# Kernel optimization log

Hardware: AMD Instinct MI355X
Metric: run time of the kernel (lower is better)

Reference implementation:

```python
import jax, jax.numpy as jnp
import numpy as np
import math

NH, NKV, D = 32, 8, 128  # query heads, kv heads, head_dim
ROPE_THETA = 10000.0


def _rotate_half(x):
    x1, x2 = jnp.split(x, 2, axis=-1)
    return jnp.concatenate([-x2, x1], axis=-1)


def _rope_cache(position_ids):
    # position_ids: [B, S] int -> cos, sin: [B, S, D]
    inv_freq = 1.0 / (ROPE_THETA ** (jnp.arange(0, D, 2, dtype=jnp.float32) / D))
    freqs = position_ids.astype(jnp.float32)[..., None] * inv_freq  # [B,S,D/2]
    emb = jnp.concatenate([freqs, freqs], axis=-1)  # [B,S,D]
    return jnp.cos(emb), jnp.sin(emb)


def setup_inputs() -> dict:
    key = jax.random.key(0)
    k0, k1, k2, k3, k4 = jax.random.split(key, 5)
    B, S, H = 1, 2048, 4096
    scale = 0.02
    return {
        "hidden_states": jax.random.normal(k0, (B, S, H), jnp.float32),
        "position_ids": jnp.broadcast_to(jnp.arange(S, dtype=jnp.int32), (B, S)),
        "Wq": jax.random.normal(k1, (H, NH * D), jnp.float32) * scale,
        "Wk": jax.random.normal(k2, (H, NKV * D), jnp.float32) * scale,
        "Wv": jax.random.normal(k3, (H, NKV * D), jnp.float32) * scale,
        "Wo": jax.random.normal(k4, (NH * D, H), jnp.float32) * scale,
    }


def reference(hidden_states, position_ids, Wq, Wk, Wv, Wo):
    B, S, H = hidden_states.shape
    # QKV projections, move heads front: [B, H, S, D]
    Q = (hidden_states @ Wq).reshape(B, S, NH, D).transpose(0, 2, 1, 3)
    K = (hidden_states @ Wk).reshape(B, S, NKV, D).transpose(0, 2, 1, 3)
    V = (hidden_states @ Wv).reshape(B, S, NKV, D).transpose(0, 2, 1, 3)
    # RoPE
    cos, sin = _rope_cache(position_ids)  # [B,S,D]
    cos, sin = cos[:, None], sin[:, None]  # broadcast over heads
    Q = Q * cos + _rotate_half(Q) * sin
    K = K * cos + _rotate_half(K) * sin
    # GQA: repeat kv heads to match query heads
    g = NH // NKV
    K = jnp.repeat(K, g, axis=1)
    V = jnp.repeat(V, g, axis=1)
    # scaled QK^T with causal mask (mask=True -> keep, else finfo.min)
    scores = jnp.einsum("bhqd,bhkd->bhqk", Q, K) / math.sqrt(D)
    causal = jnp.tril(jnp.ones((S, S), dtype=bool))
    scores = jnp.where(causal, scores, jnp.finfo(scores.dtype).min)
    probs = jax.nn.softmax(scores.astype(jnp.float32), axis=-1).astype(Q.dtype)
    attn = jnp.einsum("bhqk,bhkd->bhqd", probs, V)
    attn = attn.transpose(0, 2, 1, 3).reshape(B, S, NH * D)
    return attn @ Wo
```

## Files before the change

kernel.cpp:

```cpp
#include <hip/hip_runtime.h>
#include <hip/hip_bf16.h>
#include <math.h>

typedef __bf16 bf16;
typedef __bf16 bf16x4 __attribute__((ext_vector_type(4)));
typedef __bf16 bf16x8 __attribute__((ext_vector_type(8)));
typedef float f32x4 __attribute__((ext_vector_type(4)));

#define GLB __attribute__((address_space(1)))
#define LDSAS __attribute__((address_space(3)))

__global__ void probe_dtype(const unsigned int* __restrict__ X, int* __restrict__ flag) {
  int t = threadIdx.x;
  int cnt = 0;
  for (int i = t; i < 512; i += 64) {
    unsigned int e = (X[i] >> 7) & 0xFF;
    cnt += (e >= 110 && e <= 135) ? 1 : 0;
  }
#pragma unroll
  for (int off = 32; off > 0; off >>= 1) cnt += __shfl_down(cnt, off, 64);
  if (t == 0) flag[0] = (cnt < 256) ? 1 : 0;
}

__global__ void prep_weights(const void* __restrict__ Wq, const void* __restrict__ Wk,
                             const void* __restrict__ Wv, const void* __restrict__ Wo,
                             const void* __restrict__ X,
                             bf16* __restrict__ Wqkvt, bf16* __restrict__ Wot,
                             bf16* __restrict__ Xb, const int* __restrict__ flag) {
  const int f = flag[0];
  const int t = threadIdx.x;
  int b = blockIdx.x;
  __shared__ __attribute__((aligned(16))) bf16 tileT[64][72];
  const void* W;
  bf16* out;
  int N, bx, by;
  if (b < 4096) {
    W = Wq; out = Wqkvt; N = 4096; bx = b & 63; by = b >> 6;
  } else if (b < 5120) {
    b -= 4096; W = Wk; out = Wqkvt + (size_t)4096 * 4096; N = 1024; bx = b & 15; by = b >> 4;
  } else if (b < 6144) {
    b -= 5120; W = Wv; out = Wqkvt + (size_t)5120 * 4096; N = 1024; bx = b & 15; by = b >> 4;
  } else if (b < 10240) {
    b -= 6144; W = Wo; out = Wot; N = 4096; bx = b & 63; by = b >> 6;
  } else {
    b -= 10240;
    const size_t i = ((size_t)b * 256 + t) * 4;
    bf16x4 o;
    if (f) {
      const float4 v = *(const float4*)((const float*)X + i);
      o[0] = (bf16)v.x; o[1] = (bf16)v.y; o[2] = (bf16)v.z; o[3] = (bf16)v.w;
    } else {
      o = *(const bf16x4*)((const bf16*)X + i);
    }
    *(bf16x4*)&Xb[i] = o;
    return;
  }
  const int n0 = bx * 64, k0 = by * 64;

  const int rr = t >> 4, cc = (t & 15) * 4;
  const int s_in = (t & 15) >> 1;
#pragma unroll
  for (int p = 0; p < 4; ++p) {
    const int r = p * 16 + rr;
    bf16 vals[4];
    if (f) {
      const float4 v = *(const float4*)((const float*)W + (size_t)(k0 + r) * N + n0 + cc);
      vals[0] = (bf16)v.x; vals[1] = (bf16)v.y; vals[2] = (bf16)v.z; vals[3] = (bf16)v.w;
    } else {
      const bf16x4 v = *(const bf16x4*)((const bf16*)W + (size_t)(k0 + r) * N + n0 + cc);
#pragma unroll
      for (int u = 0; u < 4; ++u) vals[u] = v[u];
    }
    const int idx = (((r >> 3) ^ s_in) << 3) + (r & 7);
#pragma unroll
    for (int u = 0; u < 4; ++u) tileT[cc + u][idx] = vals[u];
  }
  __syncthreads();

  const int nn = t >> 3, c8 = t & 7;
#pragma unroll
  for (int p = 0; p < 2; ++p) {
    const int n = p * 32 + nn;
    const int s = (n >> 3) & 7;
    const bf16x8 v = *(const bf16x8*)&tileT[n][(c8 ^ s) * 8];
    *(bf16x8*)&out[(size_t)(n0 + n) * 4096 + k0 + c8 * 8] = v;
  }
}

__global__ __launch_bounds__(256, 2) void gemm_bt(
    const bf16* __restrict__ A, const bf16* __restrict__ Bt,
    void* __restrict__ C, const int* __restrict__ flagp, int M, int N, int K) {
  __shared__ bf16 As[128 * 64];
  __shared__ bf16 Bs[128 * 64];
  const int t = threadIdx.x;
  const int m0 = blockIdx.y * 128, n0 = blockIdx.x * 128;
  const int lane = t & 63, n16 = lane & 15, quad = lane >> 4;
  const int w = t >> 6, wrow = w >> 1, wcol = w & 1;

  f32x4 acc[4][4] = {};
  const int rA = t >> 3;
  const int colA = ((t & 7) ^ (rA & 7)) * 8;

  for (int k0 = 0; k0 < K; k0 += 64) {
#pragma unroll
    for (int i = 0; i < 4; ++i) {
      const int elem = i * 2048 + t * 8;
      const int row = i * 32 + rA;
      __builtin_amdgcn_global_load_lds(
          (const GLB void*)(A + (size_t)(m0 + row) * K + k0 + colA),
          (LDSAS void*)(&As[elem]), 16, 0, 0);
      __builtin_amdgcn_global_load_lds(
          (const GLB void*)(Bt + (size_t)(n0 + row) * K + k0 + colA),
          (LDSAS void*)(&Bs[elem]), 16, 0, 0);
    }
    __syncthreads();
#pragma unroll
    for (int kk = 0; kk < 2; ++kk) {
      bf16x8 af[4], bfr[4];
#pragma unroll
      for (int i = 0; i < 4; ++i) {
        const int rowa = wrow * 64 + i * 16 + n16;
        af[i] = *(const bf16x8*)&As[rowa * 64 + (((kk * 4 + quad) ^ (rowa & 7)) * 8)];
        const int rowb = wcol * 64 + i * 16 + n16;
        bfr[i] = *(const bf16x8*)&Bs[rowb * 64 + (((kk * 4 + quad) ^ (rowb & 7)) * 8)];
      }
#pragma unroll
      for (int mi = 0; mi < 4; ++mi)
#pragma unroll
        for (int ni = 0; ni < 4; ++ni)
          acc[mi][ni] = __builtin_amdgcn_mfma_f32_16x16x32_bf16(
              af[mi], bfr[ni], acc[mi][ni], 0, 0, 0);
    }
    __syncthreads();
  }
  const bool f32out = (flagp != nullptr) && (flagp[0] != 0);
  if (f32out) {
    float* Cf = (float*)C;
#pragma unroll
    for (int mi = 0; mi < 4; ++mi)
#pragma unroll
      for (int ni = 0; ni < 4; ++ni) {
        const int r0 = m0 + wrow * 64 + mi * 16 + quad * 4;
        const int c = n0 + wcol * 64 + ni * 16 + n16;
#pragma unroll
        for (int r = 0; r < 4; ++r) Cf[(size_t)(r0 + r) * N + c] = acc[mi][ni][r];
      }
  } else {
    bf16* Cb = (bf16*)C;
#pragma unroll
    for (int mi = 0; mi < 4; ++mi)
#pragma unroll
      for (int ni = 0; ni < 4; ++ni) {
        const int r0 = m0 + wrow * 64 + mi * 16 + quad * 4;
        const int c = n0 + wcol * 64 + ni * 16 + n16;
#pragma unroll
        for (int r = 0; r < 4; ++r) Cb[(size_t)(r0 + r) * N + c] = (bf16)acc[mi][ni][r];
      }
  }
}

__global__ void rope_vt(bf16* __restrict__ QKV, const int* __restrict__ pos,
                        bf16* __restrict__ Vt) {
  const int t = threadIdx.x;
  int b = blockIdx.x;
  if (b < 512) {
    const int i = t & 63;
    const int s = b * 4 + (t >> 6);
    const float p = (float)pos[s];
    const float inv = exp2f((float)i * -0.2076205088f);
    float sn, cs;
    sincosf(p * inv, &sn, &cs);
    bf16* base = QKV + (size_t)s * 6144 + i;
#pragma unroll 4
    for (int hh = 0; hh < 40; ++hh) {
      bf16* px = base + hh * 128;
      const float x1 = (float)px[0], x2 = (float)px[64];
      px[0] = (bf16)(x1 * cs - x2 * sn);
      px[64] = (bf16)(x2 * cs + x1 * sn);
    }
  } else {
    b -= 512;
    __shared__ bf16 tile[32][34];
    const int tx = t & 31, ty = t >> 5;
    const int v0 = (b & 31) * 32, s0 = (b >> 5) * 32;
#pragma unroll
    for (int j = 0; j < 4; ++j)
      tile[ty + j * 8][tx] = QKV[(size_t)(s0 + ty + j * 8) * 6144 + 5120 + v0 + tx];
    __syncthreads();
#pragma unroll
    for (int j = 0; j < 4; ++j)
      Vt[(size_t)(v0 + ty + j * 8) * 2048 + s0 + tx] = tile[tx][ty + j * 8];
  }
}

__global__ __launch_bounds__(256) void flash_attn(
    const bf16* __restrict__ QKV, const bf16* __restrict__ Vt_g,
    bf16* __restrict__ O) {
  __shared__ bf16 Ks[2][64 * 128];
  __shared__ bf16 Vs[2][128 * 64];
  __shared__ bf16 Ps[64 * 72];
  const int pairp = blockIdx.x;
  const int h = blockIdx.y, hkv = h >> 2;
  const int t = threadIdx.x, w = t >> 6, lane = t & 63;
  const int n16 = lane & 15, quad = lane >> 4;
  const bf16* Qp = QKV + h * 128;
  const bf16* Kp = QKV + 4096 + hkv * 128;
  const bf16* Vp = Vt_g + (size_t)hkv * 128 * 2048;

  const int krow = t >> 4, kg = t & 15;
  const int vd = t >> 3, vg = t & 7;

  for (int pass = 0; pass < 2; ++pass) {
    const int qt = (pass == 0) ? pairp : 31 - pairp;
    bf16x8 qa[4];
    {
      const bf16* qrow = Qp + (size_t)(qt * 64 + w * 16 + n16) * 6144 + quad * 8;
#pragma unroll
      for (int kf = 0; kf < 4; ++kf) qa[kf] = *(const bf16x8*)(qrow + kf * 32);
    }
    f32x4 o[8] = {};
    float l_ = 0.f;

    __syncthreads();

    auto stage = [&](int kt, int buf) {
#pragma unroll
      for (int j = 0; j < 4; ++j) {
        const int row = j * 16 + krow;
        const int g = kg ^ (row & 7);
        __builtin_amdgcn_global_load_lds(
            (const GLB void*)(Kp + (size_t)(kt * 64 + row) * 6144 + g * 8),
            (LDSAS void*)(&Ks[buf][j * 2048 + t * 8]), 16, 0, 0);
      }
#pragma unroll
      for (int j = 0; j < 4; ++j) {
        const int d = j * 32 + vd;
        const int g = vg ^ (d & 7);
        __builtin_amdgcn_global_load_lds(
            (const GLB void*)(Vp + (size_t)d * 2048 + kt * 64 + g * 8),
            (LDSAS void*)(&Vs[buf][j * 2048 + t * 8]), 16, 0, 0);
      }
    };

    stage(0, 0);
    for (int kt = 0; kt <= qt; ++kt) {
      const int cur = kt & 1;
      __syncthreads();
      if (kt < qt) stage(kt + 1, cur ^ 1);

      const bool diag = (kt == qt);
      const int s7 = n16 & 7;
      const int qloc = w * 16 + n16;
#pragma unroll
      for (int ns = 0; ns < 4; ++ns) {
        f32x4 c = {};
        __builtin_amdgcn_s_setprio(1);
#pragma unroll
        for (int kf = 0; kf < 4; ++kf)
          c = __builtin_amdgcn_mfma_f32_16x16x32_bf16(
              *(const bf16x8*)&Ks[cur][(ns * 16 + n16) * 128 +
                                       (((kf * 4 + quad) ^ s7) * 8)],
              qa[kf], c, 0, 0, 0);
        __builtin_amdgcn_s_setprio(0);
        float p[4];
        if (diag) {
          const int kv0 = ns * 16 + quad * 4;
#pragma unroll
          for (int r = 0; r < 4; ++r)
            p[r] = (kv0 + r > qloc)
                       ? 0.f
                       : __expf(fminf(c[r] * 0.08838834764831845f, 60.f));
        } else {
#pragma unroll
          for (int r = 0; r < 4; ++r)
            p[r] = __expf(fminf(c[r] * 0.08838834764831845f, 60.f));
        }
        l_ += (p[0] + p[1]) + (p[2] + p[3]);
        bf16x4 pb;
#pragma unroll
        for (int r = 0; r < 4; ++r) pb[r] = (bf16)p[r];
        *(bf16x4*)&Ps[(size_t)qloc * 72 + ns * 16 + quad * 4] = pb;
      }
      const bf16x8 a0 = *(const bf16x8*)&Ps[(w * 16 + n16) * 72 + quad * 8];
      const bf16x8 a1 = *(const bf16x8*)&Ps[(w * 16 + n16) * 72 + 32 + quad * 8];
      __builtin_amdgcn_s_setprio(1);
#pragma unroll
      for (int dt = 0; dt < 8; ++dt) {
        const int d = dt * 16 + n16;
        const bf16x8 b0 = *(const bf16x8*)&Vs[cur][d * 64 + ((quad ^ s7) * 8)];
        o[dt] = __builtin_amdgcn_mfma_f32_16x16x32_bf16(a0, b0, o[dt], 0, 0, 0);
        const bf16x8 b1 = *(const bf16x8*)&Vs[cur][d * 64 + (((4 + quad) ^ s7) * 8)];
        o[dt] = __builtin_amdgcn_mfma_f32_16x16x32_bf16(a1, b1, o[dt], 0, 0, 0);
      }
      __builtin_amdgcn_s_setprio(0);
    }
    l_ += __shfl_xor(l_, 16, 64);
    l_ += __shfl_xor(l_, 32, 64);
    float linv[4];
#pragma unroll
    for (int r = 0; r < 4; ++r) linv[r] = 1.f / __shfl(l_, quad * 4 + r, 64);
#pragma unroll
    for (int dt = 0; dt < 8; ++dt)
#pragma unroll
      for (int r = 0; r < 4; ++r) {
        const int qi = qt * 64 + w * 16 + quad * 4 + r;
        O[(size_t)qi * 4096 + h * 128 + dt * 16 + n16] = (bf16)(o[dt][r] * linv[r]);
      }
  }
}

extern "C" void kernel_launch(void* const* d_in, const int* in_sizes, int n_in,
                              void* d_out, int out_size, void* d_ws, size_t ws_size,
                              hipStream_t stream) {
  (void)in_sizes; (void)n_in; (void)out_size; (void)ws_size;
  const void* X = d_in[0];
  const int* pos = (const int*)d_in[1];
  const void* Wq = d_in[2];
  const void* Wk = d_in[3];
  const void* Wv = d_in[4];
  const void* Wo = d_in[5];

  char* ws = (char*)d_ws;
  const size_t MB = 1ull << 20;
  int* flag   = (int*)(ws + 0);
  bf16* Xb    = (bf16*)(ws + 1 * MB);
  bf16* attn  = (bf16*)(ws + 1 * MB);
  bf16* Wqkvt = (bf16*)(ws + 17 * MB);
  bf16* Wot   = (bf16*)(ws + 65 * MB);
  bf16* QKV   = (bf16*)(ws + 97 * MB);
  bf16* Vt_g  = (bf16*)(ws + 121 * MB);

  probe_dtype<<<1, 64, 0, stream>>>((const unsigned int*)X, flag);

  prep_weights<<<18432, 256, 0, stream>>>(Wq, Wk, Wv, Wo, X, Wqkvt, Wot, Xb, flag);

  gemm_bt<<<dim3(48, 16), 256, 0, stream>>>(Xb, Wqkvt, QKV, nullptr, 2048, 6144, 4096);

  rope_vt<<<2560, 256, 0, stream>>>(QKV, pos, Vt_g);

  flash_attn<<<dim3(16, 32), 256, 0, stream>>>(QKV, Vt_g, attn);

  gemm_bt<<<dim3(32, 16), 256, 0, stream>>>(attn, Wot, d_out, flag, 2048, 4096, 4096);
}
```

Baseline: 475.2 us.

## Fuse RoPE into QKV GEMM epilogue and make flash attention single-wave

```diff
diff --git a/kernel.cpp b/kernel.cpp
--- a/kernel.cpp
+++ b/kernel.cpp
@@ -24,9 +24,10 @@
 
 __global__ void prep_weights(const void* __restrict__ Wq, const void* __restrict__ Wk,
                              const void* __restrict__ Wv, const void* __restrict__ Wo,
-                             const void* __restrict__ X,
+                             const void* __restrict__ X, const int* __restrict__ pos,
                              bf16* __restrict__ Wqkvt, bf16* __restrict__ Wot,
-                             bf16* __restrict__ Xb, const int* __restrict__ flag) {
+                             bf16* __restrict__ Xb, float2* __restrict__ tab,
+                             const int* __restrict__ flag) {
   const int f = flag[0];
   const int t = threadIdx.x;
   int b = blockIdx.x;
@@ -42,7 +43,7 @@
     b -= 5120; W = Wv; out = Wqkvt + (size_t)5120 * 4096; N = 1024; bx = b & 15; by = b >> 4;
   } else if (b < 10240) {
     b -= 6144; W = Wo; out = Wot; N = 4096; bx = b & 63; by = b >> 6;
-  } else {
+  } else if (b < 18432) {
     b -= 10240;
     const size_t i = ((size_t)b * 256 + t) * 4;
     bf16x4 o;
@@ -54,6 +55,16 @@
     }
     *(bf16x4*)&Xb[i] = o;
     return;
+  } else {
+    b -= 18432;
+    const int i = t & 63;
+    const int s = b * 4 + (t >> 6);
+    const float p = (float)pos[s];
+    const float inv = exp2f((float)i * -0.2076205088f);
+    float sn, cs;
+    sincosf(p * inv, &sn, &cs);
+    tab[s * 64 + i] = make_float2(cs, sn);
+    return;
   }
   const int n0 = bx * 64, k0 = by * 64;
 
@@ -89,7 +100,8 @@
 
 __global__ __launch_bounds__(256, 2) void gemm_bt(
     const bf16* __restrict__ A, const bf16* __restrict__ Bt,
-    void* __restrict__ C, const int* __restrict__ flagp, int M, int N, int K) {
+    void* __restrict__ C, const int* __restrict__ flagp, int M, int N, int K,
+    const float2* __restrict__ tab, int rope_nbx) {
   __shared__ bf16 As[128 * 64];
   __shared__ bf16 Bs[128 * 64];
   const int t = threadIdx.x;
@@ -121,7 +133,7 @@
       for (int i = 0; i < 4; ++i) {
         const int rowa = wrow * 64 + i * 16 + n16;
         af[i] = *(const bf16x8*)&As[rowa * 64 + (((kk * 4 + quad) ^ (rowa & 7)) * 8)];
-        const int rowb = wcol * 64 + i * 16 + n16;
+        const int rowb = i * 32 + wcol * 16 + n16;
         bfr[i] = *(const bf16x8*)&Bs[rowb * 64 + (((kk * 4 + quad) ^ (rowb & 7)) * 8)];
       }
 #pragma unroll
@@ -133,6 +145,27 @@
     }
     __syncthreads();
   }
+
+  if (blockIdx.x < rope_nbx) {
+    const int i1 = wcol * 16 + n16;
+#pragma unroll
+    for (int mi = 0; mi < 4; ++mi) {
+      const int r0 = m0 + wrow * 64 + mi * 16 + quad * 4;
+#pragma unroll
+      for (int r = 0; r < 4; ++r) {
+        const int s = r0 + r;
+        const float2 cs1 = tab[s * 64 + i1];
+        const float2 cs2 = tab[s * 64 + i1 + 32];
+        const float a0 = acc[mi][0][r], a1 = acc[mi][1][r];
+        const float a2 = acc[mi][2][r], a3 = acc[mi][3][r];
+        acc[mi][0][r] = a0 * cs1.x - a2 * cs1.y;
+        acc[mi][2][r] = a2 * cs1.x + a0 * cs1.y;
+        acc[mi][1][r] = a1 * cs2.x - a3 * cs2.y;
+        acc[mi][3][r] = a3 * cs2.x + a1 * cs2.y;
+      }
+    }
+  }
+
   const bool f32out = (flagp != nullptr) && (flagp[0] != 0);
   if (f32out) {
     float* Cf = (float*)C;
@@ -141,7 +174,7 @@
 #pragma unroll
       for (int ni = 0; ni < 4; ++ni) {
         const int r0 = m0 + wrow * 64 + mi * 16 + quad * 4;
-        const int c = n0 + wcol * 64 + ni * 16 + n16;
+        const int c = n0 + ni * 32 + wcol * 16 + n16;
 #pragma unroll
         for (int r = 0; r < 4; ++r) Cf[(size_t)(r0 + r) * N + c] = acc[mi][ni][r];
       }
@@ -152,116 +185,70 @@
 #pragma unroll
       for (int ni = 0; ni < 4; ++ni) {
         const int r0 = m0 + wrow * 64 + mi * 16 + quad * 4;
-        const int c = n0 + wcol * 64 + ni * 16 + n16;
+        const int c = n0 + ni * 32 + wcol * 16 + n16;
 #pragma unroll
         for (int r = 0; r < 4; ++r) Cb[(size_t)(r0 + r) * N + c] = (bf16)acc[mi][ni][r];
       }
   }
 }
 
-__global__ void rope_vt(bf16* __restrict__ QKV, const int* __restrict__ pos,
-                        bf16* __restrict__ Vt) {
+__global__ void vt_kern(const bf16* __restrict__ QKV, bf16* __restrict__ Vt) {
   const int t = threadIdx.x;
-  int b = blockIdx.x;
-  if (b < 512) {
-    const int i = t & 63;
-    const int s = b * 4 + (t >> 6);
-    const float p = (float)pos[s];
-    const float inv = exp2f((float)i * -0.2076205088f);
-    float sn, cs;
-    sincosf(p * inv, &sn, &cs);
-    bf16* base = QKV + (size_t)s * 6144 + i;
-#pragma unroll 4
-    for (int hh = 0; hh < 40; ++hh) {
-      bf16* px = base + hh * 128;
-      const float x1 = (float)px[0], x2 = (float)px[64];
-      px[0] = (bf16)(x1 * cs - x2 * sn);
-      px[64] = (bf16)(x2 * cs + x1 * sn);
-    }
-  } else {
-    b -= 512;
-    __shared__ bf16 tile[32][34];
-    const int tx = t & 31, ty = t >> 5;
-    const int v0 = (b & 31) * 32, s0 = (b >> 5) * 32;
-#pragma unroll
-    for (int j = 0; j < 4; ++j)
-      tile[ty + j * 8][tx] = QKV[(size_t)(s0 + ty + j * 8) * 6144 + 5120 + v0 + tx];
-    __syncthreads();
-#pragma unroll
-    for (int j = 0; j < 4; ++j)
-      Vt[(size_t)(v0 + ty + j * 8) * 2048 + s0 + tx] = tile[tx][ty + j * 8];
-  }
-}
-
-__global__ __launch_bounds__(256) void flash_attn(
+  const int b = blockIdx.x;
+  __shared__ bf16 tile[32][34];
+  const int tx = t & 31, ty = t >> 5;
+  const int v0 = (b & 31) * 32, s0 = (b >> 5) * 32;
+#pragma unroll
+  for (int j = 0; j < 4; ++j)
+    tile[ty + j * 8][tx] = QKV[(size_t)(s0 + ty + j * 8) * 6144 + 5120 + v0 + tx];
+  __syncthreads();
+#pragma unroll
+  for (int j = 0; j < 4; ++j)
+    Vt[(size_t)(v0 + ty + j * 8) * 2048 + s0 + tx] = tile[tx][ty + j * 8];
+}
+
+__global__ __launch_bounds__(64) void flash_attn(
     const bf16* __restrict__ QKV, const bf16* __restrict__ Vt_g,
     bf16* __restrict__ O) {
-  __shared__ bf16 Ks[2][64 * 128];
-  __shared__ bf16 Vs[2][128 * 64];
-  __shared__ bf16 Ps[64 * 72];
-  const int pairp = blockIdx.x;
-  const int h = blockIdx.y, hkv = h >> 2;
-  const int t = threadIdx.x, w = t >> 6, lane = t & 63;
-  const int n16 = lane & 15, quad = lane >> 4;
+  __shared__ bf16 Ps[16 * 72];
+  const int bid = blockIdx.x;
+  const int xcd = bid & 7;
+  const int idx = bid >> 3;
+  const int h = xcd * 4 + (idx >> 6);
+  const int pairp = (idx >> 2) & 15;
+  const int wsub = idx & 3;
+  const int hkv = h >> 2;
+  const int t = threadIdx.x;
+  const int n16 = t & 15, quad = t >> 4;
   const bf16* Qp = QKV + h * 128;
   const bf16* Kp = QKV + 4096 + hkv * 128;
   const bf16* Vp = Vt_g + (size_t)hkv * 128 * 2048;
 
-  const int krow = t >> 4, kg = t & 15;
-  const int vd = t >> 3, vg = t & 7;
-
   for (int pass = 0; pass < 2; ++pass) {
     const int qt = (pass == 0) ? pairp : 31 - pairp;
+    const int qloc = wsub * 16 + n16;
     bf16x8 qa[4];
     {
-      const bf16* qrow = Qp + (size_t)(qt * 64 + w * 16 + n16) * 6144 + quad * 8;
+      const bf16* qrow = Qp + (size_t)(qt * 64 + qloc) * 6144 + quad * 8;
 #pragma unroll
       for (int kf = 0; kf < 4; ++kf) qa[kf] = *(const bf16x8*)(qrow + kf * 32);
     }
     f32x4 o[8] = {};
     float l_ = 0.f;
 
-    __syncthreads();
-
-    auto stage = [&](int kt, int buf) {
-#pragma unroll
-      for (int j = 0; j < 4; ++j) {
-        const int row = j * 16 + krow;
-        const int g = kg ^ (row & 7);
-        __builtin_amdgcn_global_load_lds(
-            (const GLB void*)(Kp + (size_t)(kt * 64 + row) * 6144 + g * 8),
-            (LDSAS void*)(&Ks[buf][j * 2048 + t * 8]), 16, 0, 0);
-      }
-#pragma unroll
-      for (int j = 0; j < 4; ++j) {
-        const int d = j * 32 + vd;
-        const int g = vg ^ (d & 7);
-        __builtin_amdgcn_global_load_lds(
-            (const GLB void*)(Vp + (size_t)d * 2048 + kt * 64 + g * 8),
-            (LDSAS void*)(&Vs[buf][j * 2048 + t * 8]), 16, 0, 0);
-      }
-    };
-
-    stage(0, 0);
     for (int kt = 0; kt <= qt; ++kt) {
-      const int cur = kt & 1;
-      __syncthreads();
-      if (kt < qt) stage(kt + 1, cur ^ 1);
-
+      const bf16* Kt = Kp + (size_t)(kt * 64) * 6144;
+      const bf16* Vt = Vp + kt * 64;
       const bool diag = (kt == qt);
-      const int s7 = n16 & 7;
-      const int qloc = w * 16 + n16;
 #pragma unroll
       for (int ns = 0; ns < 4; ++ns) {
         f32x4 c = {};
-        __builtin_amdgcn_s_setprio(1);
 #pragma unroll
         for (int kf = 0; kf < 4; ++kf)
           c = __builtin_amdgcn_mfma_f32_16x16x32_bf16(
-              *(const bf16x8*)&Ks[cur][(ns * 16 + n16) * 128 +
-                                       (((kf * 4 + quad) ^ s7) * 8)],
+              *(const bf16x8*)(Kt + (size_t)(ns * 16 + n16) * 6144 +
+                               (kf * 4 + quad) * 8),
               qa[kf], c, 0, 0, 0);
-        __builtin_amdgcn_s_setprio(0);
         float p[4];
         if (diag) {
           const int kv0 = ns * 16 + quad * 4;
@@ -279,20 +266,18 @@
         bf16x4 pb;
 #pragma unroll
         for (int r = 0; r < 4; ++r) pb[r] = (bf16)p[r];
-        *(bf16x4*)&Ps[(size_t)qloc * 72 + ns * 16 + quad * 4] = pb;
-      }
-      const bf16x8 a0 = *(const bf16x8*)&Ps[(w * 16 + n16) * 72 + quad * 8];
-      const bf16x8 a1 = *(const bf16x8*)&Ps[(w * 16 + n16) * 72 + 32 + quad * 8];
-      __builtin_amdgcn_s_setprio(1);
+        *(bf16x4*)&Ps[n16 * 72 + ns * 16 + quad * 4] = pb;
+      }
+      const bf16x8 a0 = *(const bf16x8*)&Ps[n16 * 72 + quad * 8];
+      const bf16x8 a1 = *(const bf16x8*)&Ps[n16 * 72 + 32 + quad * 8];
 #pragma unroll
       for (int dt = 0; dt < 8; ++dt) {
-        const int d = dt * 16 + n16;
-        const bf16x8 b0 = *(const bf16x8*)&Vs[cur][d * 64 + ((quad ^ s7) * 8)];
+        const bf16* vr = Vt + (size_t)(dt * 16 + n16) * 2048;
+        const bf16x8 b0 = *(const bf16x8*)(vr + quad * 8);
         o[dt] = __builtin_amdgcn_mfma_f32_16x16x32_bf16(a0, b0, o[dt], 0, 0, 0);
-        const bf16x8 b1 = *(const bf16x8*)&Vs[cur][d * 64 + (((4 + quad) ^ s7) * 8)];
+        const bf16x8 b1 = *(const bf16x8*)(vr + 32 + quad * 8);
         o[dt] = __builtin_amdgcn_mfma_f32_16x16x32_bf16(a1, b1, o[dt], 0, 0, 0);
       }
-      __builtin_amdgcn_s_setprio(0);
     }
     l_ += __shfl_xor(l_, 16, 64);
     l_ += __shfl_xor(l_, 32, 64);
@@ -303,7 +288,7 @@
     for (int dt = 0; dt < 8; ++dt)
 #pragma unroll
       for (int r = 0; r < 4; ++r) {
-        const int qi = qt * 64 + w * 16 + quad * 4 + r;
+        const int qi = qt * 64 + wsub * 16 + quad * 4 + r;
         O[(size_t)qi * 4096 + h * 128 + dt * 16 + n16] = (bf16)(o[dt][r] * linv[r]);
       }
   }
@@ -322,23 +307,27 @@
 
   char* ws = (char*)d_ws;
   const size_t MB = 1ull << 20;
-  int* flag   = (int*)(ws + 0);
-  bf16* Xb    = (bf16*)(ws + 1 * MB);
-  bf16* attn  = (bf16*)(ws + 1 * MB);
-  bf16* Wqkvt = (bf16*)(ws + 17 * MB);
-  bf16* Wot   = (bf16*)(ws + 65 * MB);
-  bf16* QKV   = (bf16*)(ws + 97 * MB);
-  bf16* Vt_g  = (bf16*)(ws + 121 * MB);
+  int* flag     = (int*)(ws + 0);
+  bf16* Xb      = (bf16*)(ws + 1 * MB);
+  bf16* attn    = (bf16*)(ws + 1 * MB);
+  bf16* Wqkvt   = (bf16*)(ws + 17 * MB);
+  bf16* Wot     = (bf16*)(ws + 65 * MB);
+  bf16* QKV     = (bf16*)(ws + 97 * MB);
+  bf16* Vt_g    = (bf16*)(ws + 121 * MB);
+  float2* tab   = (float2*)(ws + 121 * MB);
 
   probe_dtype<<<1, 64, 0, stream>>>((const unsigned int*)X, flag);
 
-  prep_weights<<<18432, 256, 0, stream>>>(Wq, Wk, Wv, Wo, X, Wqkvt, Wot, Xb, flag);
-
-  gemm_bt<<<dim3(48, 16), 256, 0, stream>>>(Xb, Wqkvt, QKV, nullptr, 2048, 6144, 4096);
-
-  rope_vt<<<2560, 256, 0, stream>>>(QKV, pos, Vt_g);
-
-  flash_attn<<<dim3(16, 32), 256, 0, stream>>>(QKV, Vt_g, attn);
-
-  gemm_bt<<<dim3(32, 16), 256, 0, stream>>>(attn, Wot, d_out, flag, 2048, 4096, 4096);
-}
+  prep_weights<<<18944, 256, 0, stream>>>(Wq, Wk, Wv, Wo, X, pos,
+                                          Wqkvt, Wot, Xb, tab, flag);
+
+  gemm_bt<<<dim3(48, 16), 256, 0, stream>>>(Xb, Wqkvt, QKV, nullptr,
+                                            2048, 6144, 4096, tab, 40);
+
+  vt_kern<<<2048, 256, 0, stream>>>(QKV, Vt_g);
+
+  flash_attn<<<2048, 64, 0, stream>>>(QKV, Vt_g, attn);
+
+  gemm_bt<<<dim3(32, 16), 256, 0, stream>>>(attn, Wot, d_out, flag,
+                                            2048, 4096, 4096, tab, 0);
+}
```

Result: slower. 664.6 us (+39.9%).
